# Kernel optimization log

Hardware: AMD Instinct MI355X
Metric: run time of the kernel (lower is better)

The kernel has to match this reference:

```python
import jax, jax.numpy as jnp
import numpy as np

EPS = 1e-4  # IRLS smoothing epsilon

def _corr(x, k):
    # x: [C,H,W], k: [kh,kw]; cross-correlation, 'same' output, replicate (clamp) boundary
    ph, pw = k.shape[0] // 2, k.shape[1] // 2
    xp = jnp.pad(x, ((0, 0), (ph, ph), (pw, pw)), mode='edge')
    out = jax.lax.conv_general_dilated(xp[:, None], k[None, None].astype(x.dtype), (1, 1), 'VALID', dimension_numbers=('NCHW', 'OIHW', 'NCHW'))
    return out[:, 0]

def _flip(k):
    return k[::-1, ::-1]

def _forward(blurred, kernel, reg_kernels, reg_kernel_weights, reg_target_kernels, reg_powers, num_irls_iter, num_cg_iter):
    n = reg_kernels.shape[0]
    w_kernel = jnp.ones_like(blurred)                       # data-term weights (ones, as in forward)
    w_reg = jnp.ones((n,) + blurred.shape, blurred.dtype)   # IRLS reg weights, start at 1
    lam = reg_kernel_weights ** 2                           # squared weights keep A PSD

    def R(x, ks):  # apply each reg kernel -> [N,C,H,W]
        return jax.vmap(lambda k: _corr(x, k))(ks)

    def RT(y, ks):  # adjoint: correlate with flipped kernels, y: [N,C,H,W]
        return jax.vmap(lambda yi, k: _corr(yi, _flip(k)))(y, ks)

    def A(x, w_reg):  # A = K^T W K + sum_n lam_n R_n^T W_n R_n
        data = _corr(w_kernel * _corr(x, kernel), _flip(kernel))
        reg = jnp.einsum('n,nchw->chw', lam, RT(w_reg * R(x, reg_kernels), reg_kernels))
        return data + reg

    Tb = R(blurred, reg_target_kernels)           # regularization targets T_n b
    KtWb = _corr(w_kernel * blurred, _flip(kernel))
    x0 = blurred
    for _ in range(num_irls_iter):
        # DeconvCGInit: rhs and initial residual/search direction
        rhs = KtWb + jnp.einsum('n,nchw->chw', lam, RT(w_reg * Tb, reg_kernels))
        x = x0
        r = rhs - A(x, w_reg)
        p = r
        # DeconvCGIter: standard CG updates
        for _ in range(num_cg_iter):
            Ap = A(p, w_reg)
            rr = jnp.sum(r * r)
            alpha = rr / jnp.sum(p * Ap)
            x = x + alpha * p
            r = r - alpha * Ap
            beta = jnp.sum(r * r) / rr
            p = r + beta * p
        x0 = x
        # DeconvCGWeight: IRLS reweighting w_n = p_n * (|R_n x - T_n b| + eps)^(p_n - 2)
        d = R(x0, reg_kernels) - Tb
        pw = reg_powers[:, None, None, None]
        w_reg = pw * jnp.power(jnp.abs(d) + EPS, pw - 2.0)
    return x0

def setup_inputs():
    key = jax.random.key(0)
    ks = jax.random.split(key, 6)
    C, H, W = 3, 1024, 1024
    NREG, RKS, BKS = 5, 5, 15
    blurred = jax.random.uniform(ks[0], (C, H, W), jnp.float32)
    kernel = jax.random.uniform(ks[1], (BKS, BKS), jnp.float32)
    kernel = kernel / jnp.sum(kernel)  # normalized blur kernel
    rk = 0.1 * jax.random.normal(ks[2], (NREG, RKS, RKS), jnp.float32)
    rk = rk.at[0, 2, 2].add(-2.0).at[0, 3, 2].add(1.0).at[0, 2, 3].add(1.0)  # gradient stencil init
    rkw = 0.1 * jax.random.normal(ks[3], (NREG,), jnp.float32)
    rkw = rkw.at[0].add(1.0)
    rtk = 0.1 * jax.random.normal(ks[4], (NREG, RKS, RKS), jnp.float32)
    rp = 1.0 + 0.02 * jax.random.normal(ks[5], (NREG,), jnp.float32)
    return {"blurred": blurred, "kernel": kernel, "reg_kernels": rk, "reg_kernel_weights": rkw, "reg_target_kernels": rtk, "reg_powers": rp, "num_irls_iter": 2, "num_cg_iter": 4}

def reference(blurred, kernel, reg_kernels, reg_kernel_weights, reg_target_kernels, reg_powers, num_irls_iter, num_cg_iter):
    return _forward(blurred, kernel, reg_kernels, reg_kernel_weights, reg_target_kernels, reg_powers, num_irls_iter, num_cg_iter)
```

## Files before the change

### kernel.cpp

```cpp
#include <hip/hip_runtime.h>
#include <math.h>

#define HH 1024
#define WW 1024
#define CHN 3
#define PLANE (HH*WW)
#define IMG (CHN*PLANE)
#define NREG 5
#define EPSV 1e-4f

#define OFF_WREG 0
#define OFF_KTWB (5*IMG)
#define OFF_T    (6*IMG)
#define OFF_R    (7*IMG)
#define OFF_P    (8*IMG)
#define OFF_AP   (9*IMG)
#define OFF_PART (10*IMG)

__global__ __launch_bounds__(256) void k_init(const float4* __restrict__ b,
                                              float4* __restrict__ x) {
  const int stride = gridDim.x * 256;
  for (int i = blockIdx.x * 256 + threadIdx.x; i < IMG / 4; i += stride)
    x[i] = b[i];
}

template <bool FLIP>
__global__ __launch_bounds__(256) void k_corr15(const float* __restrict__ in,
                                                const float* __restrict__ k15,
                                                float* __restrict__ out) {
  __shared__ float tile[78 * 87];
  __shared__ float kpad[15 * 16];
  const int ch = blockIdx.z;
  const int R0 = blockIdx.y * 64;
  const int C0 = blockIdx.x * 72;
  const int tid = threadIdx.x;
  if (tid < 240) {
    int a = tid >> 4, b = tid & 15;
    float v = 0.f;
    if (b < 15) v = FLIP ? k15[(14 - a) * 15 + (14 - b)] : k15[a * 15 + b];
    kpad[tid] = v;
  }
  const float* inc = in + ch * PLANE;
  for (int i = tid; i < 78 * 86; i += 256) {
    int r = i / 86, c = i - r * 86;
    int gr = min(max(R0 - 7 + r, 0), HH - 1);
    int gc = min(max(C0 - 7 + c, 0), WW - 1);
    tile[r * 87 + c] = inc[gr * WW + gc];
  }
  __syncthreads();
  const int tx = tid & 7, ty = tid >> 3;
  const int oi = ty * 2, oj = tx * 9;
  float acc[2][9];
#pragma unroll
  for (int o = 0; o < 2; ++o)
#pragma unroll
    for (int q = 0; q < 9; ++q) acc[o][q] = 0.f;

#pragma unroll 1
  for (int rr = 0; rr < 16; ++rr) {
    float wv[23];
#pragma unroll
    for (int q = 0; q < 23; ++q) wv[q] = tile[(oi + rr) * 87 + oj + q];
#pragma unroll
    for (int o = 0; o < 2; ++o) {
      int a = rr - o;
      if ((unsigned)a < 15u) {
        const float4* kp = (const float4*)&kpad[a * 16];
        float4 kA = kp[0], kB = kp[1], kC = kp[2], kD = kp[3];
        float kv[16] = {kA.x, kA.y, kA.z, kA.w, kB.x, kB.y, kB.z, kB.w,
                        kC.x, kC.y, kC.z, kC.w, kD.x, kD.y, kD.z, kD.w};
#pragma unroll
        for (int b = 0; b < 15; ++b)
#pragma unroll
          for (int q = 0; q < 9; ++q)
            acc[o][q] = fmaf(kv[b], wv[b + q], acc[o][q]);
      }
    }
  }
  float* oc = out + ch * PLANE;
#pragma unroll
  for (int o = 0; o < 2; ++o) {
    const int orow = R0 + oi + o;
#pragma unroll
    for (int q = 0; q < 9; ++q) {
      int gcol = C0 + oj + q;
      if (gcol < WW) oc[orow * WW + gcol] = acc[o][q];
    }
  }
}

__device__ __forceinline__ void blk_reduce2(float a, float b, float* scratch,
                                            float* o1, float* o2) {
#pragma unroll
  for (int off = 32; off > 0; off >>= 1) {
    a += __shfl_down(a, off, 64);
    b += __shfl_down(b, off, 64);
  }
  __syncthreads();
  const int lane = threadIdx.x & 63, wid = threadIdx.x >> 6;
  if (lane == 0) { scratch[wid] = a; scratch[4 + wid] = b; }
  __syncthreads();
  if (threadIdx.x == 0) {
    *o1 = scratch[0] + scratch[1] + scratch[2] + scratch[3];
    *o2 = scratch[4] + scratch[5] + scratch[6] + scratch[7];
  }
}

template <int MODE, bool W1>
__global__ __launch_bounds__(256) void k_reg(
    const float* __restrict__ src, const float* __restrict__ kin_all,
    const float* __restrict__ rk, const float* __restrict__ rkw,
    const float* __restrict__ wreg, const float* __restrict__ ktwb,
    float* __restrict__ ap, const float* __restrict__ rin,
    float* __restrict__ rout, float* __restrict__ pout,
    float* __restrict__ part) {
  __shared__ float sbuf[40 * 73];
  __shared__ float vbuf[36 * 69];
  __shared__ float kin_s[NREG * 25];
  __shared__ float kf_s[NREG * 25];
  __shared__ float scratch[8];
  const int ch = blockIdx.z;
  const int R0 = blockIdx.y * 32, C0 = blockIdx.x * 64;
  const int tid = threadIdx.x;
  const int lane = tid & 63, wid = tid >> 6;
  const int W = wid * 8;

  if (tid < NREG * 25) {
    int n = tid / 25, j = tid - n * 25, a = j / 5, b = j - a * 5;
    kin_s[tid] = kin_all[tid];
    float lw = rkw[n];
    kf_s[tid] = lw * lw * rk[n * 25 + (4 - a) * 5 + (4 - b)];
  }
  const float* sc = src + ch * PLANE;
  for (int i = tid; i < 40 * 72; i += 256) {
    int r = i / 72, c = i - r * 72;
    int gr = min(max(R0 - 4 + r, 0), HH - 1);
    int gc = min(max(C0 - 4 + c, 0), WW - 1);
    sbuf[r * 73 + c] = sc[gr * WW + gc];
  }
  __syncthreads();

  float acc[8];
#pragma unroll
  for (int s = 0; s < 8; ++s) acc[s] = 0.f;

  for (int n = 0; n < NREG; ++n) {
    float kin[25];
#pragma unroll
    for (int j = 0; j < 25; ++j) kin[j] = kin_s[n * 25 + j];
    const float* wn = wreg + (n * CHN + ch) * PLANE;

    for (int e = tid; e < 400; e += 256) {
      int vr, vc;
      if (e < 136)      { vr = e / 68;            vc = e - (e / 68) * 68; }
      else if (e < 272) { int j2 = e - 136; vr = 34 + j2 / 68; vc = j2 - (j2 / 68) * 68; }
      else              { int j2 = e - 272; vr = 2 + (j2 >> 2);
                          int m = j2 & 3; vc = (m < 2) ? m : 64 + m; }
      int rc = min(max(R0 - 2 + vr, 0), HH - 1);
      int cc = min(max(C0 - 2 + vc, 0), WW - 1);
      int tr = rc - R0 + 4, tc = cc - C0 + 4;
      float s = 0.f;
#pragma unroll
      for (int a = 0; a < 5; ++a)
#pragma unroll
        for (int b = 0; b < 5; ++b)
          s = fmaf(kin[a * 5 + b], sbuf[(tr - 2 + a) * 73 + tc - 2 + b], s);
      vbuf[vr * 69 + vc] = W1 ? s : s * wn[rc * WW + cc];
    }

    float vacc[8];
#pragma unroll
    for (int s = 0; s < 8; ++s) vacc[s] = 0.f;
#pragma unroll
    for (int rr = 0; rr < 12; ++rr) {
      float x5[5];
#pragma unroll
      for (int b = 0; b < 5; ++b) x5[b] = sbuf[(2 + W + rr) * 73 + lane + 2 + b];
#pragma unroll
      for (int a = 0; a < 5; ++a) {
        int s = rr - a;
        if (s >= 0 && s < 8) {
#pragma unroll
          for (int b = 0; b < 5; ++b) vacc[s] = fmaf(kin[a * 5 + b], x5[b], vacc[s]);
        }
      }
    }
    if constexpr (W1) {
#pragma unroll
      for (int s = 0; s < 8; ++s)
        vbuf[(2 + W + s) * 69 + lane + 2] = vacc[s];
    } else {
#pragma unroll
      for (int s = 0; s < 8; ++s)
        vbuf[(2 + W + s) * 69 + lane + 2] = vacc[s] * wn[(R0 + W + s) * WW + C0 + lane];
    }
    __syncthreads();

    float kf[25];
#pragma unroll
    for (int j = 0; j < 25; ++j) kf[j] = kf_s[n * 25 + j];
#pragma unroll
    for (int rv = 0; rv < 12; ++rv) {
      float v5[5];
#pragma unroll
      for (int b = 0; b < 5; ++b) v5[b] = vbuf[(W + rv) * 69 + lane + b];
#pragma unroll
      for (int a = 0; a < 5; ++a) {
        int s = rv - a;
        if (s >= 0 && s < 8) {
#pragma unroll
          for (int b = 0; b < 5; ++b) acc[s] = fmaf(kf[a * 5 + b], v5[b], acc[s]);
        }
      }
    }
    __syncthreads();
  }

  const int obase = ch * PLANE + (R0 + W) * WW + C0 + lane;
  if constexpr (MODE == 2) {
#pragma unroll
    for (int s = 0; s < 8; ++s) {
      float rv = ktwb[obase + s * WW] - ap[obase + s * WW] + acc[s];
      rout[obase + s * WW] = rv;
      pout[obase + s * WW] = rv;
    }
  } else {
    float pap = 0.f, rr2 = 0.f;
#pragma unroll
    for (int s = 0; s < 8; ++s) {
      float av = ap[obase + s * WW] + acc[s];
      ap[obase + s * WW] = av;
      if constexpr (MODE == 0) {
        float pv = src[obase + s * WW];
        float rv = rin[obase + s * WW];
        pap = fmaf(av, pv, pap);
        rr2 = fmaf(rv, rv, rr2);
      }
    }
    if constexpr (MODE == 0) {
      float s1, s2;
      blk_reduce2(pap, rr2, scratch, &s1, &s2);
      if (tid == 0) {
        int bid = (blockIdx.z * 32 + blockIdx.y) * 16 + blockIdx.x;
        part[bid] = s1;
        part[2048 + bid] = s2;
      }
    }
  }
}

__global__ __launch_bounds__(256) void k_wupd(
    const float* __restrict__ x, const float* __restrict__ blur,
    const float* __restrict__ rk, const float* __restrict__ rtk,
    const float* __restrict__ rp, float* __restrict__ wreg) {
  __shared__ float xb[68 * 69];
  __shared__ float bb[68 * 69];
  __shared__ float k1s[NREG * 25], k2s[NREG * 25];
  __shared__ float rps[NREG];
  const int ch = blockIdx.z, R0 = blockIdx.y * 64, C0 = blockIdx.x * 64;
  const int tid = threadIdx.x;
  const int lane = tid & 63, wid = tid >> 6, W = wid * 16;
  if (tid < NREG * 25) { k1s[tid] = rk[tid]; k2s[tid] = rtk[tid]; }
  if (tid < NREG) rps[tid] = rp[tid];
  const float* xc = x + ch * PLANE;
  const float* bc = blur + ch * PLANE;
  for (int i = tid; i < 68 * 68; i += 256) {
    int r = i / 68, c = i - r * 68;
    int gr = min(max(R0 - 2 + r, 0), HH - 1);
    int gc = min(max(C0 - 2 + c, 0), WW - 1);
    xb[r * 69 + c] = xc[gr * WW + gc];
    bb[r * 69 + c] = bc[gr * WW + gc];
  }
  __syncthreads();
  for (int n = 0; n < NREG; ++n) {
    float k1[25], k2[25];
#pragma unroll
    for (int j = 0; j < 25; ++j) { k1[j] = k1s[n * 25 + j]; k2[j] = k2s[n * 25 + j]; }
    float d_[16];
#pragma unroll
    for (int s = 0; s < 16; ++s) d_[s] = 0.f;
#pragma unroll
    for (int rr = 0; rr < 20; ++rr) {
      float x5[5], b5[5];
#pragma unroll
      for (int b = 0; b < 5; ++b) {
        x5[b] = xb[(W + rr) * 69 + lane + b];
        b5[b] = bb[(W + rr) * 69 + lane + b];
      }
#pragma unroll
      for (int a = 0; a < 5; ++a) {
        int s = rr - a;
        if (s >= 0 && s < 16) {
#pragma unroll
          for (int b = 0; b < 5; ++b) {
            d_[s] = fmaf(k1[a * 5 + b], x5[b], d_[s]);
            d_[s] = fmaf(-k2[a * 5 + b], b5[b], d_[s]);
          }
        }
      }
    }
    float pw = rps[n];
    float* wc = wreg + (n * CHN + ch) * PLANE + (R0 + W) * WW + C0 + lane;
#pragma unroll
    for (int s = 0; s < 16; ++s) {
      float v = fabsf(d_[s]) + EPSV;
      wc[s * WW] = pw * __expf((pw - 2.f) * __logf(v));
    }
  }
}

__global__ __launch_bounds__(256) void k_upd_xr(
    float4* __restrict__ x, const float4* __restrict__ p,
    float4* __restrict__ r, const float4* __restrict__ ap,
    const float* __restrict__ part, float* __restrict__ part2) {
  __shared__ float scratch[8];
  __shared__ float sAlpha;
  {
    float a = 0.f, b = 0.f;
    for (int i = threadIdx.x; i < 1536; i += 256) {
      a += part[i];
      b += part[2048 + i];
    }
    float s1, s2;
    blk_reduce2(a, b, scratch, &s1, &s2);
    if (threadIdx.x == 0) sAlpha = s2 / s1;
    __syncthreads();
  }
  const float alpha = sAlpha;
  float s = 0.f;
  const int stride = gridDim.x * 256;
  for (int i = blockIdx.x * 256 + threadIdx.x; i < IMG / 4; i += stride) {
    float4 xv = x[i], pv = p[i], rv = r[i], av = ap[i];
    xv.x += alpha * pv.x; xv.y += alpha * pv.y; xv.z += alpha * pv.z; xv.w += alpha * pv.w;
    rv.x -= alpha * av.x; rv.y -= alpha * av.y; rv.z -= alpha * av.z; rv.w -= alpha * av.w;
    x[i] = xv; r[i] = rv;
    s += rv.x * rv.x + rv.y * rv.y + rv.z * rv.z + rv.w * rv.w;
  }
#pragma unroll
  for (int off = 32; off > 0; off >>= 1) s += __shfl_down(s, off, 64);
  __syncthreads();
  if ((threadIdx.x & 63) == 0) scratch[threadIdx.x >> 6] = s;
  __syncthreads();
  if (threadIdx.x == 0)
    part2[blockIdx.x] = scratch[0] + scratch[1] + scratch[2] + scratch[3];
}

__global__ __launch_bounds__(256) void k_upd_x(
    float4* __restrict__ x, const float4* __restrict__ p,
    const float* __restrict__ part) {
  __shared__ float scratch[8];
  __shared__ float sAlpha;
  {
    float a = 0.f, b = 0.f;
    for (int i = threadIdx.x; i < 1536; i += 256) {
      a += part[i];
      b += part[2048 + i];
    }
    float s1, s2;
    blk_reduce2(a, b, scratch, &s1, &s2);
    if (threadIdx.x == 0) sAlpha = s2 / s1;
    __syncthreads();
  }
  const float alpha = sAlpha;
  const int stride = gridDim.x * 256;
  for (int i = blockIdx.x * 256 + threadIdx.x; i < IMG / 4; i += stride) {
    float4 xv = x[i], pv = p[i];
    xv.x += alpha * pv.x; xv.y += alpha * pv.y; xv.z += alpha * pv.z; xv.w += alpha * pv.w;
    x[i] = xv;
  }
}

__global__ __launch_bounds__(256) void k_upd_p(
    float4* __restrict__ p, const float4* __restrict__ r,
    const float* __restrict__ part, const float* __restrict__ part2) {
  __shared__ float scratch[8];
  __shared__ float sBeta;
  {
    float a = 0.f, b = 0.f;
    for (int i = threadIdx.x; i < 1536; i += 256) {
      if (i < 768) a += part2[i];
      b += part[2048 + i];
    }
    float s1, s2;
    blk_reduce2(a, b, scratch, &s1, &s2);
    if (threadIdx.x == 0) sBeta = s1 / s2;
    __syncthreads();
  }
  const float beta = sBeta;
  const int stride = gridDim.x * 256;
  for (int i = blockIdx.x * 256 + threadIdx.x; i < IMG / 4; i += stride) {
    float4 pv = p[i], rv = r[i];
    pv.x = rv.x + beta * pv.x; pv.y = rv.y + beta * pv.y;
    pv.z = rv.z + beta * pv.z; pv.w = rv.w + beta * pv.w;
    p[i] = pv;
  }
}

extern "C" void kernel_launch(void* const* d_in, const int* in_sizes, int n_in,
                              void* d_out, int out_size, void* d_ws, size_t ws_size,
                              hipStream_t stream) {
  (void)in_sizes; (void)n_in; (void)out_size; (void)ws_size;
  const float* blurred = (const float*)d_in[0];
  const float* k15 = (const float*)d_in[1];
  const float* rk  = (const float*)d_in[2];
  const float* rkw = (const float*)d_in[3];
  const float* rtk = (const float*)d_in[4];
  const float* rp  = (const float*)d_in[5];

  float* x = (float*)d_out;
  float* ws = (float*)d_ws;
  float* wreg  = ws + OFF_WREG;
  float* ktwb  = ws + OFF_KTWB;
  float* t     = ws + OFF_T;
  float* r     = ws + OFF_R;
  float* p     = ws + OFF_P;
  float* ap    = ws + OFF_AP;
  float* part  = ws + OFF_PART;
  float* part2 = part + 4096;

  const dim3 b256(256);
  const dim3 g15(15, 16, CHN);
  const dim3 gRG(16, 32, CHN);
  const dim3 g64(16, 16, CHN);

  k_init<<<dim3(768), b256, 0, stream>>>((const float4*)blurred, (float4*)x);
  k_corr15<true><<<g15, b256, 0, stream>>>(blurred, k15, ktwb);

  for (int irls = 0; irls < 2; ++irls) {
    k_corr15<false><<<g15, b256, 0, stream>>>(x, k15, t);
    k_corr15<true><<<g15, b256, 0, stream>>>(t, k15, ap);
    if (irls == 0) {
      k_reg<1, true><<<gRG, b256, 0, stream>>>(x, rk, rk, rkw, wreg, nullptr, ap,
                                               nullptr, nullptr, nullptr, nullptr);
      k_reg<2, true><<<gRG, b256, 0, stream>>>(blurred, rtk, rk, rkw, wreg, ktwb, ap,
                                               nullptr, r, p, nullptr);
    } else {
      k_reg<1, false><<<gRG, b256, 0, stream>>>(x, rk, rk, rkw, wreg, nullptr, ap,
                                                nullptr, nullptr, nullptr, nullptr);
      k_reg<2, false><<<gRG, b256, 0, stream>>>(blurred, rtk, rk, rkw, wreg, ktwb, ap,
                                                nullptr, r, p, nullptr);
    }
    for (int cg = 0; cg < 4; ++cg) {
      const bool last = (cg == 3);
      k_corr15<false><<<g15, b256, 0, stream>>>(p, k15, t);
      k_corr15<true><<<g15, b256, 0, stream>>>(t, k15, ap);
      if (irls == 0)
        k_reg<0, true><<<gRG, b256, 0, stream>>>(p, rk, rk, rkw, wreg, nullptr, ap,
                                                 r, nullptr, nullptr, part);
      else
        k_reg<0, false><<<gRG, b256, 0, stream>>>(p, rk, rk, rkw, wreg, nullptr, ap,
                                                  r, nullptr, nullptr, part);
      if (!last) {
        k_upd_xr<<<dim3(768), b256, 0, stream>>>((float4*)x, (const float4*)p,
                                                 (float4*)r, (const float4*)ap,
                                                 part, part2);
        k_upd_p<<<dim3(768), b256, 0, stream>>>((float4*)p, (const float4*)r,
                                                part, part2);
      } else {
        k_upd_x<<<dim3(768), b256, 0, stream>>>((float4*)x, (const float4*)p, part);
      }
    }
    if (irls == 0)
      k_wupd<<<g64, b256, 0, stream>>>(x, blurred, rk, rtk, rp, wreg);
  }
}
```

Baseline: 1.567 ms.

## Halve row tiles in corr15 and wupd, prefetch IRLS weights in k_reg

The 15x15 correlation kernel now computes one output row per thread over a 32-row tile instead of two rows over 64. This shrinks shared memory and accumulator registers and doubles the grid. The weight-update kernel is retiled the same way (8 rows per wave). k_reg now loads all five weight planes into registers at kernel start rather than inside the per-regularizer loop, so those global loads can overlap the tile fill. The trade-off is more redundant halo loads per output and higher register use in k_reg.

Measured after the change: 1.439 ms. -8.2%, faster.

```diff
diff --git a/kernel.cpp b/kernel.cpp
--- a/kernel.cpp
+++ b/kernel.cpp
@@ -28,10 +28,10 @@
 __global__ __launch_bounds__(256) void k_corr15(const float* __restrict__ in,
                                                 const float* __restrict__ k15,
                                                 float* __restrict__ out) {
-  __shared__ float tile[78 * 87];
+  __shared__ float tile[46 * 88];
   __shared__ float kpad[15 * 16];
   const int ch = blockIdx.z;
-  const int R0 = blockIdx.y * 64;
+  const int R0 = blockIdx.y * 32;
   const int C0 = blockIdx.x * 72;
   const int tid = threadIdx.x;
   if (tid < 240) {
@@ -41,51 +41,40 @@
     kpad[tid] = v;
   }
   const float* inc = in + ch * PLANE;
-  for (int i = tid; i < 78 * 86; i += 256) {
+  for (int i = tid; i < 46 * 86; i += 256) {
     int r = i / 86, c = i - r * 86;
     int gr = min(max(R0 - 7 + r, 0), HH - 1);
     int gc = min(max(C0 - 7 + c, 0), WW - 1);
-    tile[r * 87 + c] = inc[gr * WW + gc];
+    tile[r * 88 + c] = inc[gr * WW + gc];
   }
   __syncthreads();
   const int tx = tid & 7, ty = tid >> 3;
-  const int oi = ty * 2, oj = tx * 9;
-  float acc[2][9];
-#pragma unroll
-  for (int o = 0; o < 2; ++o)
-#pragma unroll
-    for (int q = 0; q < 9; ++q) acc[o][q] = 0.f;
+  const int oi = ty, oj = tx * 9;
+  float acc[9];
+#pragma unroll
+  for (int q = 0; q < 9; ++q) acc[q] = 0.f;
 
 #pragma unroll 1
-  for (int rr = 0; rr < 16; ++rr) {
+  for (int a = 0; a < 15; ++a) {
     float wv[23];
 #pragma unroll
-    for (int q = 0; q < 23; ++q) wv[q] = tile[(oi + rr) * 87 + oj + q];
-#pragma unroll
-    for (int o = 0; o < 2; ++o) {
-      int a = rr - o;
-      if ((unsigned)a < 15u) {
-        const float4* kp = (const float4*)&kpad[a * 16];
-        float4 kA = kp[0], kB = kp[1], kC = kp[2], kD = kp[3];
-        float kv[16] = {kA.x, kA.y, kA.z, kA.w, kB.x, kB.y, kB.z, kB.w,
-                        kC.x, kC.y, kC.z, kC.w, kD.x, kD.y, kD.z, kD.w};
-#pragma unroll
-        for (int b = 0; b < 15; ++b)
-#pragma unroll
-          for (int q = 0; q < 9; ++q)
-            acc[o][q] = fmaf(kv[b], wv[b + q], acc[o][q]);
-      }
-    }
+    for (int q = 0; q < 23; ++q) wv[q] = tile[(oi + a) * 88 + oj + q];
+    const float4* kp = (const float4*)&kpad[a * 16];
+    float4 kA = kp[0], kB = kp[1], kC = kp[2], kD = kp[3];
+    float kv[16] = {kA.x, kA.y, kA.z, kA.w, kB.x, kB.y, kB.z, kB.w,
+                    kC.x, kC.y, kC.z, kC.w, kD.x, kD.y, kD.z, kD.w};
+#pragma unroll
+    for (int b = 0; b < 15; ++b)
+#pragma unroll
+      for (int q = 0; q < 9; ++q)
+        acc[q] = fmaf(kv[b], wv[b + q], acc[q]);
   }
   float* oc = out + ch * PLANE;
-#pragma unroll
-  for (int o = 0; o < 2; ++o) {
-    const int orow = R0 + oi + o;
-#pragma unroll
-    for (int q = 0; q < 9; ++q) {
-      int gcol = C0 + oj + q;
-      if (gcol < WW) oc[orow * WW + gcol] = acc[o][q];
-    }
+  const int orow = R0 + oi;
+#pragma unroll
+  for (int q = 0; q < 9; ++q) {
+    int gcol = C0 + oj + q;
+    if (gcol < WW) oc[orow * WW + gcol] = acc[q];
   }
 }
 
@@ -125,6 +114,17 @@
   const int lane = tid & 63, wid = tid >> 6;
   const int W = wid * 8;
 
+  float wpre[NREG][8];
+  if constexpr (!W1) {
+#pragma unroll
+    for (int n = 0; n < NREG; ++n) {
+      const float* wn = wreg + (n * CHN + ch) * PLANE;
+#pragma unroll
+      for (int s = 0; s < 8; ++s)
+        wpre[n][s] = wn[(R0 + W + s) * WW + C0 + lane];
+    }
+  }
+
   if (tid < NREG * 25) {
     int n = tid / 25, j = tid - n * 25, a = j / 5, b = j - a * 5;
     kin_s[tid] = kin_all[tid];
@@ -192,7 +192,7 @@
     } else {
 #pragma unroll
       for (int s = 0; s < 8; ++s)
-        vbuf[(2 + W + s) * 69 + lane + 2] = vacc[s] * wn[(R0 + W + s) * WW + C0 + lane];
+        vbuf[(2 + W + s) * 69 + lane + 2] = vacc[s] * wpre[n][s];
     }
     __syncthreads();
 
@@ -253,18 +253,18 @@
     const float* __restrict__ x, const float* __restrict__ blur,
     const float* __restrict__ rk, const float* __restrict__ rtk,
     const float* __restrict__ rp, float* __restrict__ wreg) {
-  __shared__ float xb[68 * 69];
-  __shared__ float bb[68 * 69];
+  __shared__ float xb[36 * 69];
+  __shared__ float bb[36 * 69];
   __shared__ float k1s[NREG * 25], k2s[NREG * 25];
   __shared__ float rps[NREG];
-  const int ch = blockIdx.z, R0 = blockIdx.y * 64, C0 = blockIdx.x * 64;
+  const int ch = blockIdx.z, R0 = blockIdx.y * 32, C0 = blockIdx.x * 64;
   const int tid = threadIdx.x;
-  const int lane = tid & 63, wid = tid >> 6, W = wid * 16;
+  const int lane = tid & 63, wid = tid >> 6, W = wid * 8;
   if (tid < NREG * 25) { k1s[tid] = rk[tid]; k2s[tid] = rtk[tid]; }
   if (tid < NREG) rps[tid] = rp[tid];
   const float* xc = x + ch * PLANE;
   const float* bc = blur + ch * PLANE;
-  for (int i = tid; i < 68 * 68; i += 256) {
+  for (int i = tid; i < 36 * 68; i += 256) {
     int r = i / 68, c = i - r * 68;
     int gr = min(max(R0 - 2 + r, 0), HH - 1);
     int gc = min(max(C0 - 2 + c, 0), WW - 1);
@@ -276,11 +276,11 @@
     float k1[25], k2[25];
 #pragma unroll
     for (int j = 0; j < 25; ++j) { k1[j] = k1s[n * 25 + j]; k2[j] = k2s[n * 25 + j]; }
-    float d_[16];
-#pragma unroll
-    for (int s = 0; s < 16; ++s) d_[s] = 0.f;
-#pragma unroll
-    for (int rr = 0; rr < 20; ++rr) {
+    float d_[8];
+#pragma unroll
+    for (int s = 0; s < 8; ++s) d_[s] = 0.f;
+#pragma unroll
+    for (int rr = 0; rr < 12; ++rr) {
       float x5[5], b5[5];
 #pragma unroll
       for (int b = 0; b < 5; ++b) {
@@ -290,7 +290,7 @@
 #pragma unroll
       for (int a = 0; a < 5; ++a) {
         int s = rr - a;
-        if (s >= 0 && s < 16) {
+        if (s >= 0 && s < 8) {
 #pragma unroll
           for (int b = 0; b < 5; ++b) {
             d_[s] = fmaf(k1[a * 5 + b], x5[b], d_[s]);
@@ -302,7 +302,7 @@
     float pw = rps[n];
     float* wc = wreg + (n * CHN + ch) * PLANE + (R0 + W) * WW + C0 + lane;
 #pragma unroll
-    for (int s = 0; s < 16; ++s) {
+    for (int s = 0; s < 8; ++s) {
       float v = fabsf(d_[s]) + EPSV;
       wc[s * WW] = pw * __expf((pw - 2.f) * __logf(v));
     }
@@ -419,9 +419,9 @@
   float* part2 = part + 4096;
 
   const dim3 b256(256);
-  const dim3 g15(15, 16, CHN);
+  const dim3 g15(15, 32, CHN);
   const dim3 gRG(16, 32, CHN);
-  const dim3 g64(16, 16, CHN);
+  const dim3 gWU(16, 32, CHN);
 
   k_init<<<dim3(768), b256, 0, stream>>>((const float4*)blurred, (float4*)x);
   k_corr15<true><<<g15, b256, 0, stream>>>(blurred, k15, ktwb);
@@ -461,6 +461,6 @@
       }
     }
     if (irls == 0)
-      k_wupd<<<g64, b256, 0, stream>>>(x, blurred, rk, rtk, rp, wreg);
-  }
-}
+      k_wupd<<<gWU, b256, 0, stream>>>(x, blurred, rk, rtk, rp, wreg);
+  }
+}
```
